# Kernel optimization log

Hardware: AMD Instinct MI355X
Metric: run time of the kernel (lower is better)

The kernel has to match this reference:

```python
import jax, jax.numpy as jnp
import numpy as np

N_NODES = 50000
N_EDGES = 1_600_000
IN_CH = 128
HEADS = 4
OUT_CH = 16
NEG_SLOPE = 0.2


def setup_inputs() -> dict:
    key = jax.random.key(0)
    ks = jax.random.split(key, 6)
    x = jax.random.normal(ks[0], (N_NODES, IN_CH), dtype=jnp.float32)
    row = jax.random.randint(ks[1], (N_EDGES,), 0, N_NODES, dtype=jnp.int32)
    # offset in [1, N) guarantees no self loops in the input graph
    off = jax.random.randint(ks[2], (N_EDGES,), 1, N_NODES, dtype=jnp.int32)
    col = (row + off) % N_NODES
    edge_index = jnp.stack([row, col], axis=0)  # [2, E]
    edge_attr = jax.random.uniform(ks[3], (N_EDGES, HEADS), dtype=jnp.float32)
    weight = jax.random.normal(ks[4], (IN_CH, HEADS * OUT_CH), dtype=jnp.float32) * (1.0 / np.sqrt(IN_CH))
    att_weight = jax.random.normal(ks[5], (1, HEADS, 2 * OUT_CH), dtype=jnp.float32) * 0.1
    bias = jnp.zeros((HEADS * OUT_CH,), dtype=jnp.float32)
    return {"x": x, "edge_index": edge_index, "edge_attr": edge_attr,
            "weight": weight, "att_weight": att_weight, "bias": bias}


def reference(x, edge_index, edge_attr, weight, att_weight, bias):
    N = x.shape[0]
    H, C = HEADS, OUT_CH
    # linear projection: [N, in] @ [in, H*C] -> [N, H, C]
    h = (x @ weight).reshape(N, H, C)
    # add self loops (input is guaranteed self-loop free); self-loop edge_attr = 1
    loop = jnp.arange(N, dtype=edge_index.dtype)
    row = jnp.concatenate([edge_index[0], loop])
    col = jnp.concatenate([edge_index[1], loop])
    ea = jnp.concatenate([edge_attr, jnp.ones((N, H), dtype=edge_attr.dtype)], axis=0)
    edge_index_full = jnp.stack([row, col], axis=0)
    # attention score: cat([h[row], h[col]], -1) * att_weight, summed over feature dim
    a_src = att_weight[0, :, :C]   # [H, C]
    a_dst = att_weight[0, :, C:]   # [H, C]
    alpha = (jnp.einsum('ehc,hc->eh', h[row], a_src)
             + jnp.einsum('ehc,hc->eh', h[col], a_dst))  # [E+N, H]
    alpha = jnp.where(alpha >= 0, alpha, NEG_SLOPE * alpha)  # leaky_relu
    alpha = alpha * ea
    # weighted aggregation: scatter-add messages to row nodes
    msg = alpha[:, :, None] * h[col]                 # [E+N, H, C]
    out = jax.ops.segment_sum(msg, row, num_segments=N)  # [N, H, C]
    out = out.reshape(N, H * C) + bias               # concat heads
    return (out, edge_index_full, alpha)
```

## Files before the change

kernel.cpp:

```cpp
#include <hip/hip_runtime.h>

#define N_NODES 50000
#define N_EDGES 1600000
#define IN_CH 128
#define HEADS 4
#define HC 64
#define E_FULL (N_EDGES + N_NODES)
#define NEG_SLOPE 0.2f

#define BUCKET_NODES 98
#define NBUCK 512
#define BIN_TILE 2048
#define NBLK_BIN ((N_EDGES + BIN_TILE - 1) / BIN_TILE)
#define T_FLAT (NBUCK * NBLK_BIN)
#define SCANA_BLOCKS (T_FLAT / 256)

__device__ __forceinline__ float leaky(float s) { return s >= 0.f ? s : NEG_SLOPE * s; }

__device__ __forceinline__ unsigned f2bf(float f) {
    unsigned u = __float_as_uint(f);
    return (u + 0x7fffu + ((u >> 16) & 1u)) >> 16;
}
__device__ __forceinline__ float bf2f(unsigned v) {
    return __uint_as_float(v << 16);
}

__global__ __launch_bounds__(256) void gemm_h_kernel(
    const float* __restrict__ x, const float* __restrict__ weight,
    const float* __restrict__ att, unsigned short* __restrict__ h16,
    float* __restrict__ s_src, float* __restrict__ s_dst)
{
    __shared__ float w_lds[IN_CH * HC];
    __shared__ float x_lds[8 * IN_CH];
    const int tid = threadIdx.x;
    const int nbase = blockIdx.x * 8;

    for (int i = tid; i < IN_CH * HC; i += 256) w_lds[i] = weight[i];
    for (int i = tid; i < 8 * IN_CH; i += 256) {
        int n = nbase + i / IN_CH;
        x_lds[i] = (n < N_NODES) ? x[(size_t)n * IN_CH + (i % IN_CH)] : 0.f;
    }
    __syncthreads();

    const int w = tid >> 6;
    const int lane = tid & 63;
    const int n0 = nbase + w;
    const int n1 = nbase + 4 + w;

    float acc0 = 0.f, acc1 = 0.f;
    #pragma unroll 8
    for (int k = 0; k < IN_CH; ++k) {
        float wv = w_lds[k * HC + lane];
        acc0 = fmaf(x_lds[w * IN_CH + k], wv, acc0);
        acc1 = fmaf(x_lds[(w + 4) * IN_CH + k], wv, acc1);
    }

    if (n0 < N_NODES) h16[(size_t)n0 * HC + lane] = (unsigned short)f2bf(acc0);
    if (n1 < N_NODES) h16[(size_t)n1 * HC + lane] = (unsigned short)f2bf(acc1);

    const int hd = lane >> 4, c = lane & 15;
    float as = att[hd * 32 + c], ad = att[hd * 32 + 16 + c];
    float ts0 = acc0 * as, td0 = acc0 * ad;
    float ts1 = acc1 * as, td1 = acc1 * ad;
    #pragma unroll
    for (int m = 8; m >= 1; m >>= 1) {
        ts0 += __shfl_xor(ts0, m, 64);
        td0 += __shfl_xor(td0, m, 64);
        ts1 += __shfl_xor(ts1, m, 64);
        td1 += __shfl_xor(td1, m, 64);
    }
    if (c == 0) {
        if (n0 < N_NODES) { s_src[n0 * HEADS + hd] = ts0; s_dst[n0 * HEADS + hd] = td0; }
        if (n1 < N_NODES) { s_src[n1 * HEADS + hd] = ts1; s_dst[n1 * HEADS + hd] = td1; }
    }
}

__global__ __launch_bounds__(256) void histM_kernel(
    const int* __restrict__ ei, unsigned* __restrict__ M,
    float* __restrict__ eif)
{
    __shared__ unsigned lh[NBUCK];
    const int tid = threadIdx.x;
    for (int j = tid; j < NBUCK; j += 256) lh[j] = 0;
    __syncthreads();
    const int base = blockIdx.x * BIN_TILE;
    #pragma unroll
    for (int k = 0; k < 8; ++k) {
        int e = base + k * 256 + tid;
        if (e < N_EDGES) {
            unsigned r = (unsigned)ei[e];
            unsigned c = (unsigned)ei[N_EDGES + e];
            eif[e] = (float)r;
            eif[(size_t)E_FULL + e] = (float)c;
            atomicAdd(&lh[r / BUCKET_NODES], 1u);
        }
    }
    __syncthreads();
    unsigned* Mb = M + (size_t)blockIdx.x * NBUCK;
    for (int j = tid; j < NBUCK; j += 256) Mb[j] = lh[j];
}

__device__ __forceinline__ unsigned block_excl_scan(unsigned v, unsigned* total,
                                                    int tid) {
    const int lane = tid & 63, wid = tid >> 6;
    unsigned x = v;
    #pragma unroll
    for (int d = 1; d < 64; d <<= 1) {
        unsigned t = __shfl_up(x, d, 64);
        if (lane >= d) x += t;
    }
    __shared__ unsigned wsum[4];
    if (lane == 63) wsum[wid] = x;
    __syncthreads();
    unsigned woff = 0;
    for (int i = 0; i < wid; ++i) woff += wsum[i];
    unsigned incl = x + woff;
    if (tid == 255) *total = incl;
    return incl - v;
}

__global__ __launch_bounds__(256) void scanA_kernel(
    const unsigned* __restrict__ M, unsigned* __restrict__ localx,
    unsigned* __restrict__ partials)
{
    const int tid = threadIdx.x;
    const int f = blockIdx.x * 256 + tid;
    unsigned v = 0;
    if (f < T_FLAT) {
        int bucket = f / NBLK_BIN;
        int blk = f - bucket * NBLK_BIN;
        v = M[(size_t)blk * NBUCK + bucket];
    }
    __shared__ unsigned tot;
    unsigned excl = block_excl_scan(v, &tot, tid);
    if (f < T_FLAT) localx[f] = excl;
    __syncthreads();
    if (tid == 0) partials[blockIdx.x] = tot;
}

__global__ __launch_bounds__(256) void scanB_kernel(
    const unsigned* __restrict__ partials, unsigned* __restrict__ pscan)
{
    __shared__ unsigned tot_sh;
    __shared__ unsigned carry_sh;
    const int tid = threadIdx.x;
    if (tid == 0) carry_sh = 0;
    __syncthreads();
    const int nchunk = (SCANA_BLOCKS + 255) / 256;
    for (int ch = 0; ch < nchunk; ++ch) {
        int i = ch * 256 + tid;
        unsigned v = (i < SCANA_BLOCKS) ? partials[i] : 0u;
        unsigned excl = block_excl_scan(v, &tot_sh, tid);
        unsigned carry = carry_sh;
        if (i < SCANA_BLOCKS) pscan[i] = excl + carry;
        __syncthreads();
        if (tid == 0) carry_sh += tot_sh;
        __syncthreads();
    }
}

__global__ __launch_bounds__(256) void scanC_kernel(
    const unsigned* __restrict__ localx, const unsigned* __restrict__ pscan,
    unsigned* __restrict__ S)
{
    const int f = blockIdx.x * 256 + threadIdx.x;
    if (f < T_FLAT) S[f] = localx[f] + pscan[blockIdx.x];
    if (f == 0) S[T_FLAT] = N_EDGES;
}

__global__ __launch_bounds__(256) void bin_kernel(
    const int* __restrict__ ei, const float* __restrict__ ea,
    const float* __restrict__ s_src, const float* __restrict__ s_dst,
    const unsigned* __restrict__ S, uint4* __restrict__ slots,
    float* __restrict__ alpha)
{
    __shared__ unsigned lh[NBUCK];
    __shared__ unsigned lbase[NBUCK];
    const int tid = threadIdx.x;
    for (int j = tid; j < NBUCK; j += 256) lh[j] = 0;
    __syncthreads();

    const int base = blockIdx.x * BIN_TILE;
    unsigned b8[8], idx8[8], p0[8], p1[8], p2[8];
    #pragma unroll
    for (int k = 0; k < 8; ++k) {
        int e = base + k * 256 + tid;
        b8[k] = 0xffffffffu;
        if (e < N_EDGES) {
            unsigned r = (unsigned)ei[e];
            unsigned c = (unsigned)ei[N_EDGES + e];
            float4 ss = ((const float4*)s_src)[r];
            float4 sd = ((const float4*)s_dst)[c];
            float4 eav = ((const float4*)ea)[e];
            float4 a;
            a.x = leaky(ss.x + sd.x) * eav.x;
            a.y = leaky(ss.y + sd.y) * eav.y;
            a.z = leaky(ss.z + sd.z) * eav.z;
            a.w = leaky(ss.w + sd.w) * eav.w;
            ((float4*)alpha)[e] = a;

            unsigned bk = r / BUCKET_NODES;
            unsigned rl = r - bk * BUCKET_NODES;
            b8[k] = bk;
            p0[k] = c | (rl << 16);
            p1[k] = f2bf(a.x) | (f2bf(a.y) << 16);
            p2[k] = f2bf(a.z) | (f2bf(a.w) << 16);
            idx8[k] = atomicAdd(&lh[bk], 1u);
        }
    }
    __syncthreads();
    for (int j = tid; j < NBUCK; j += 256)
        lbase[j] = S[(size_t)j * NBLK_BIN + blockIdx.x];
    __syncthreads();
    #pragma unroll
    for (int k = 0; k < 8; ++k) {
        if (b8[k] != 0xffffffffu)
            slots[lbase[b8[k]] + idx8[k]] = make_uint4(p0[k], p1[k], p2[k], 0u);
    }
}

__global__ __launch_bounds__(256) void sort_kernel(
    const unsigned* __restrict__ S, const uint4* __restrict__ slots,
    uint4* __restrict__ slots2, unsigned* __restrict__ offs)
{
    __shared__ unsigned cnt[BUCKET_NODES];
    __shared__ unsigned cur[BUCKET_NODES];
    const int b = blockIdx.x;
    const int tid = threadIdx.x;
    const unsigned start = S[(size_t)b * NBLK_BIN];
    const unsigned end   = S[(size_t)(b + 1) * NBLK_BIN];

    for (int j = tid; j < BUCKET_NODES; j += 256) cnt[j] = 0;
    __syncthreads();
    for (unsigned i = start + tid; i < end; i += 256)
        atomicAdd(&cnt[slots[i].x >> 16], 1u);
    __syncthreads();
    if (tid == 0) {
        unsigned run = 0;
        for (int j = 0; j < BUCKET_NODES; ++j) {
            unsigned c = cnt[j];
            cur[j] = run;
            run += c;
        }
    }
    __syncthreads();
    const int nstart = b * BUCKET_NODES;
    for (int j = tid; j < BUCKET_NODES; j += 256) {
        int n = nstart + j;
        if (n <= N_NODES) offs[n] = start + cur[j];
    }
    __syncthreads();
    for (unsigned i = start + tid; i < end; i += 256) {
        uint4 s = slots[i];
        unsigned rl = s.x >> 16;
        unsigned pos = start + atomicAdd(&cur[rl], 1u);
        slots2[pos] = s;
    }
}

__device__ __forceinline__ float slot_alpha(uint4 s, int hd) {
    unsigned w = (hd & 2) ? s.z : s.y;
    return bf2f((hd & 1) ? (w >> 16) : (w & 0xffffu));
}

__global__ __launch_bounds__(256) void gather_kernel(
    const unsigned short* __restrict__ h16, const float* __restrict__ s_src,
    const float* __restrict__ s_dst, const float* __restrict__ bias,
    const unsigned* __restrict__ offs, const uint4* __restrict__ slots2,
    float* __restrict__ alpha, float* __restrict__ out, float* __restrict__ eif)
{
    const int tid = threadIdx.x;
    const int n = blockIdx.x * 4 + (tid >> 6);
    if (n >= N_NODES) return;
    const int lane = tid & 63, hd = lane >> 4;

    float s_self = s_src[n * HEADS + hd] + s_dst[n * HEADS + hd];
    float acc = bias[lane] + leaky(s_self) * bf2f(h16[(size_t)n * HC + lane]);

    const unsigned start = offs[n];
    const int cnt = (int)(offs[n + 1] - start);

    int i = 0;
    for (; i + 3 < cnt; i += 4) {
        uint4 s0 = slots2[start + i];
        uint4 s1 = slots2[start + i + 1];
        uint4 s2 = slots2[start + i + 2];
        uint4 s3 = slots2[start + i + 3];
        float h0 = bf2f(h16[(size_t)(s0.x & 0xffffu) * HC + lane]);
        float h1 = bf2f(h16[(size_t)(s1.x & 0xffffu) * HC + lane]);
        float h2 = bf2f(h16[(size_t)(s2.x & 0xffffu) * HC + lane]);
        float h3 = bf2f(h16[(size_t)(s3.x & 0xffffu) * HC + lane]);
        acc = fmaf(slot_alpha(s0, hd), h0, acc);
        acc = fmaf(slot_alpha(s1, hd), h1, acc);
        acc = fmaf(slot_alpha(s2, hd), h2, acc);
        acc = fmaf(slot_alpha(s3, hd), h3, acc);
    }
    for (; i < cnt; ++i) {
        uint4 s0 = slots2[start + i];
        float h0 = bf2f(h16[(size_t)(s0.x & 0xffffu) * HC + lane]);
        acc = fmaf(slot_alpha(s0, hd), h0, acc);
    }
    out[(size_t)n * HC + lane] = acc;

    if (lane < HEADS) {
        float s2 = s_src[n * HEADS + lane] + s_dst[n * HEADS + lane];
        alpha[(size_t)(N_EDGES + n) * HEADS + lane] = leaky(s2);
    }
    if (lane == 4) eif[N_EDGES + n] = (float)n;
    if (lane == 5) eif[(size_t)E_FULL + N_EDGES + n] = (float)n;
}

extern "C" void kernel_launch(void* const* d_in, const int* in_sizes, int n_in,
                              void* d_out, int out_size, void* d_ws, size_t ws_size,
                              hipStream_t stream) {
    const float* x      = (const float*)d_in[0];
    const int*   ei     = (const int*)  d_in[1];
    const float* ea     = (const float*)d_in[2];
    const float* weight = (const float*)d_in[3];
    const float* att    = (const float*)d_in[4];
    const float* bias   = (const float*)d_in[5];

    float* out   = (float*)d_out;
    float* eif   = out + (size_t)N_NODES * HC;
    float* alpha = eif + (size_t)2 * E_FULL;

    uint4* slots  = (uint4*)d_ws;
    uint4* slots2 = slots + (size_t)N_EDGES;
    unsigned short* h16 = (unsigned short*)(slots2 + (size_t)N_EDGES);
    float* s_src = (float*)(h16 + (size_t)N_NODES * HC);
    float* s_dst = s_src + (size_t)N_NODES * HEADS;
    unsigned* M        = (unsigned*)(s_dst + (size_t)N_NODES * HEADS);
    unsigned* localx   = M + (size_t)NBLK_BIN * NBUCK;
    unsigned* partials = localx + T_FLAT;
    unsigned* pscan    = partials + SCANA_BLOCKS;
    unsigned* S        = pscan + SCANA_BLOCKS;
    unsigned* offs     = S + (T_FLAT + 1);

    gemm_h_kernel<<<(N_NODES + 7) / 8, 256, 0, stream>>>(x, weight, att, h16, s_src, s_dst);
    histM_kernel<<<NBLK_BIN, 256, 0, stream>>>(ei, M, eif);
    scanA_kernel<<<SCANA_BLOCKS, 256, 0, stream>>>(M, localx, partials);
    scanB_kernel<<<1, 256, 0, stream>>>(partials, pscan);
    scanC_kernel<<<SCANA_BLOCKS, 256, 0, stream>>>(localx, pscan, S);
    bin_kernel<<<NBLK_BIN, 256, 0, stream>>>(ei, ea, s_src, s_dst, S, slots, alpha);
    sort_kernel<<<NBUCK, 256, 0, stream>>>(S, slots, slots2, offs);
    gather_kernel<<<(N_NODES + 3) / 4, 256, 0, stream>>>(
        h16, s_src, s_dst, bias, offs, slots2, alpha, out, eif);
}
```

Before: 183.1 us.

## Compute node projection with bf16 MFMA and deepen gather unroll to eight

Replaces the scalar FP32 LDS-based projection GEMM with a bf16 MFMA 16x16x32 kernel. A new small kernel pre-converts and transposes the weight to bf16. Each block now covers 64 nodes, with x converted to bf16 into a swizzled LDS tile, which cuts the per-block weight reload and the FMA work. The gather loop is also unrolled from 4 to 8 edges so more independent loads are in flight. The trade-off is lower GEMM input precision from bf16 inputs and one extra tiny kernel launch.

Measured after the change: 167.5 us. -8.5%, faster.

```diff
diff --git a/kernel.cpp b/kernel.cpp
--- a/kernel.cpp
+++ b/kernel.cpp
@@ -15,6 +15,9 @@
 #define T_FLAT (NBUCK * NBLK_BIN)
 #define SCANA_BLOCKS (T_FLAT / 256)
 
+typedef __attribute__((ext_vector_type(8))) short short8v;
+typedef __attribute__((ext_vector_type(4))) float float4v;
+
 __device__ __forceinline__ float leaky(float s) { return s >= 0.f ? s : NEG_SLOPE * s; }
 
 __device__ __forceinline__ unsigned f2bf(float f) {
@@ -25,53 +28,93 @@
     return __uint_as_float(v << 16);
 }
 
+__global__ __launch_bounds__(256) void wcvt_kernel(
+    const float* __restrict__ w, unsigned short* __restrict__ wT)
+{
+    int i = blockIdx.x * 256 + threadIdx.x;
+    if (i < IN_CH * HC) {
+        int k = i >> 6, c = i & 63;
+        wT[c * IN_CH + k] = (unsigned short)f2bf(w[i]);
+    }
+}
+
 __global__ __launch_bounds__(256) void gemm_h_kernel(
-    const float* __restrict__ x, const float* __restrict__ weight,
+    const float* __restrict__ x, const unsigned short* __restrict__ wT,
     const float* __restrict__ att, unsigned short* __restrict__ h16,
     float* __restrict__ s_src, float* __restrict__ s_dst)
 {
-    __shared__ float w_lds[IN_CH * HC];
-    __shared__ float x_lds[8 * IN_CH];
-    const int tid = threadIdx.x;
-    const int nbase = blockIdx.x * 8;
-
-    for (int i = tid; i < IN_CH * HC; i += 256) w_lds[i] = weight[i];
-    for (int i = tid; i < 8 * IN_CH; i += 256) {
-        int n = nbase + i / IN_CH;
-        x_lds[i] = (n < N_NODES) ? x[(size_t)n * IN_CH + (i % IN_CH)] : 0.f;
-    }
-    __syncthreads();
-
-    const int w = tid >> 6;
-    const int lane = tid & 63;
-    const int n0 = nbase + w;
-    const int n1 = nbase + 4 + w;
-
-    float acc0 = 0.f, acc1 = 0.f;
-    #pragma unroll 8
-    for (int k = 0; k < IN_CH; ++k) {
-        float wv = w_lds[k * HC + lane];
-        acc0 = fmaf(x_lds[w * IN_CH + k], wv, acc0);
-        acc1 = fmaf(x_lds[(w + 4) * IN_CH + k], wv, acc1);
-    }
-
-    if (n0 < N_NODES) h16[(size_t)n0 * HC + lane] = (unsigned short)f2bf(acc0);
-    if (n1 < N_NODES) h16[(size_t)n1 * HC + lane] = (unsigned short)f2bf(acc1);
-
-    const int hd = lane >> 4, c = lane & 15;
-    float as = att[hd * 32 + c], ad = att[hd * 32 + 16 + c];
-    float ts0 = acc0 * as, td0 = acc0 * ad;
-    float ts1 = acc1 * as, td1 = acc1 * ad;
-    #pragma unroll
-    for (int m = 8; m >= 1; m >>= 1) {
-        ts0 += __shfl_xor(ts0, m, 64);
-        td0 += __shfl_xor(td0, m, 64);
-        ts1 += __shfl_xor(ts1, m, 64);
-        td1 += __shfl_xor(td1, m, 64);
-    }
-    if (c == 0) {
-        if (n0 < N_NODES) { s_src[n0 * HEADS + hd] = ts0; s_dst[n0 * HEADS + hd] = td0; }
-        if (n1 < N_NODES) { s_src[n1 * HEADS + hd] = ts1; s_dst[n1 * HEADS + hd] = td1; }
+    __shared__ unsigned short x_lds[64 * 128];
+    const int tid = threadIdx.x;
+    const int nbase = blockIdx.x * 64;
+
+    #pragma unroll
+    for (int s = 0; s < 8; ++s) {
+        int i = s * 256 + tid;
+        int node = i >> 5;
+        int q = i & 31;
+        float4 v = make_float4(0.f, 0.f, 0.f, 0.f);
+        int gn = nbase + node;
+        if (gn < N_NODES) v = ((const float4*)x)[(size_t)gn * 32 + q];
+        ushort4 b;
+        b.x = (unsigned short)f2bf(v.x);
+        b.y = (unsigned short)f2bf(v.y);
+        b.z = (unsigned short)f2bf(v.z);
+        b.w = (unsigned short)f2bf(v.w);
+        int chunk = q >> 1, half = q & 1;
+        int sw = chunk ^ (node & 7);
+        *(ushort4*)&x_lds[node * 128 + sw * 8 + half * 4] = b;
+    }
+    __syncthreads();
+
+    const int wid = tid >> 6, lane = tid & 63;
+    const int g = lane >> 4, m = lane & 15;
+    const int rt = wid;
+
+    float4v acc[4] = {{0.f,0.f,0.f,0.f},{0.f,0.f,0.f,0.f},
+                      {0.f,0.f,0.f,0.f},{0.f,0.f,0.f,0.f}};
+    #pragma unroll
+    for (int kk = 0; kk < 4; ++kk) {
+        int chunk = (kk * 4 + g) ^ (m & 7);
+        short8v a = *(const short8v*)&x_lds[(rt * 16 + m) * 128 + chunk * 8];
+        #pragma unroll
+        for (int ct = 0; ct < 4; ++ct) {
+            short8v bfr = *(const short8v*)&wT[(ct * 16 + m) * IN_CH + kk * 32 + g * 8];
+            acc[ct] = __builtin_amdgcn_mfma_f32_16x16x32_bf16(a, bfr, acc[ct], 0, 0, 0);
+        }
+    }
+
+    #pragma unroll
+    for (int ct = 0; ct < 4; ++ct) {
+        float as = att[ct * 32 + m];
+        float ad = att[ct * 32 + 16 + m];
+        float ts[4], td[4];
+        #pragma unroll
+        for (int r = 0; r < 4; ++r) {
+            int node = nbase + rt * 16 + g * 4 + r;
+            float v = acc[ct][r];
+            if (node < N_NODES)
+                h16[(size_t)node * HC + ct * 16 + m] = (unsigned short)f2bf(v);
+            ts[r] = v * as;
+            td[r] = v * ad;
+        }
+        #pragma unroll
+        for (int msk = 1; msk <= 8; msk <<= 1) {
+            #pragma unroll
+            for (int r = 0; r < 4; ++r) {
+                ts[r] += __shfl_xor(ts[r], msk, 64);
+                td[r] += __shfl_xor(td[r], msk, 64);
+            }
+        }
+        if (m == 0) {
+            #pragma unroll
+            for (int r = 0; r < 4; ++r) {
+                int node = nbase + rt * 16 + g * 4 + r;
+                if (node < N_NODES) {
+                    s_src[node * HEADS + ct] = ts[r];
+                    s_dst[node * HEADS + ct] = td[r];
+                }
+            }
+        }
     }
 }
 
@@ -281,19 +324,17 @@
     const int cnt = (int)(offs[n + 1] - start);
 
     int i = 0;
-    for (; i + 3 < cnt; i += 4) {
-        uint4 s0 = slots2[start + i];
-        uint4 s1 = slots2[start + i + 1];
-        uint4 s2 = slots2[start + i + 2];
-        uint4 s3 = slots2[start + i + 3];
-        float h0 = bf2f(h16[(size_t)(s0.x & 0xffffu) * HC + lane]);
-        float h1 = bf2f(h16[(size_t)(s1.x & 0xffffu) * HC + lane]);
-        float h2 = bf2f(h16[(size_t)(s2.x & 0xffffu) * HC + lane]);
-        float h3 = bf2f(h16[(size_t)(s3.x & 0xffffu) * HC + lane]);
-        acc = fmaf(slot_alpha(s0, hd), h0, acc);
-        acc = fmaf(slot_alpha(s1, hd), h1, acc);
-        acc = fmaf(slot_alpha(s2, hd), h2, acc);
-        acc = fmaf(slot_alpha(s3, hd), h3, acc);
+    for (; i + 7 < cnt; i += 8) {
+        uint4 sl[8];
+        float hv[8];
+        #pragma unroll
+        for (int u = 0; u < 8; ++u) sl[u] = slots2[start + i + u];
+        #pragma unroll
+        for (int u = 0; u < 8; ++u)
+            hv[u] = bf2f(h16[(size_t)(sl[u].x & 0xffffu) * HC + lane]);
+        #pragma unroll
+        for (int u = 0; u < 8; ++u)
+            acc = fmaf(slot_alpha(sl[u], hd), hv[u], acc);
     }
     for (; i < cnt; ++i) {
         uint4 s0 = slots2[start + i];
@@ -326,7 +367,8 @@
 
     uint4* slots  = (uint4*)d_ws;
     uint4* slots2 = slots + (size_t)N_EDGES;
-    unsigned short* h16 = (unsigned short*)(slots2 + (size_t)N_EDGES);
+    unsigned short* wT = (unsigned short*)(slots2 + (size_t)N_EDGES);
+    unsigned short* h16 = wT + (size_t)IN_CH * HC;
     float* s_src = (float*)(h16 + (size_t)N_NODES * HC);
     float* s_dst = s_src + (size_t)N_NODES * HEADS;
     unsigned* M        = (unsigned*)(s_dst + (size_t)N_NODES * HEADS);
@@ -336,7 +378,8 @@
     unsigned* S        = pscan + SCANA_BLOCKS;
     unsigned* offs     = S + (T_FLAT + 1);
 
-    gemm_h_kernel<<<(N_NODES + 7) / 8, 256, 0, stream>>>(x, weight, att, h16, s_src, s_dst);
+    wcvt_kernel<<<(IN_CH * HC + 255) / 256, 256, 0, stream>>>(weight, wT);
+    gemm_h_kernel<<<(N_NODES + 63) / 64, 256, 0, stream>>>(x, wT, att, h16, s_src, s_dst);
     histM_kernel<<<NBLK_BIN, 256, 0, stream>>>(ei, M, eif);
     scanA_kernel<<<SCANA_BLOCKS, 256, 0, stream>>>(M, localx, partials);
     scanB_kernel<<<1, 256, 0, stream>>>(partials, pscan);
```
